# Optimization experiments

Measured on AMD Instinct MI355X. Metric: run time of the kernel, lower is better.

## Reference

```python
import jax, jax.numpy as jnp
import numpy as np

N = 100_000      # nodes
E = 1_600_000    # edges (avg degree 16)
D = 64           # input_dim == hidden_dim
C = 10           # output classes
G = 512          # graphs in batch
L = 5            # num_layers (L-1 = 4 GINConv layers)
BN_EPS = 1e-5


def setup_inputs() -> dict:
    key = jax.random.key(0)
    ks = jax.random.split(key, 16)
    x = jax.random.normal(ks[0], (N, D), dtype=jnp.float32)
    edge_index = jax.random.randint(ks[1], (2, E), 0, N, dtype=jnp.int32)
    batch = jnp.sort(jax.random.randint(ks[2], (N,), 0, G, dtype=jnp.int32))
    s = 1.0 / np.sqrt(D)
    Lc = L - 1
    return {
        "x": x,
        "edge_index": edge_index,
        "batch": batch,
        "eps": jnp.zeros((Lc,), jnp.float32),                                   # GINConv eps (train_eps, init 0)
        "W1": jax.random.uniform(ks[3], (Lc, D, D), jnp.float32, -s, s),        # MLP linear 1
        "b1": jax.random.uniform(ks[4], (Lc, D), jnp.float32, -s, s),
        "g1": jnp.ones((Lc, D), jnp.float32),                                   # MLP BatchNorm
        "be1": jnp.zeros((Lc, D), jnp.float32),
        "W2": jax.random.uniform(ks[5], (Lc, D, D), jnp.float32, -s, s),        # MLP linear 2
        "b2": jax.random.uniform(ks[6], (Lc, D), jnp.float32, -s, s),
        "gout": jnp.ones((Lc, D), jnp.float32),                                 # outer BatchNorm
        "beout": jnp.zeros((Lc, D), jnp.float32),
        "Wp": jax.random.uniform(ks[7], (L, D, C), jnp.float32, -s, s),         # prediction linears
        "bp": jax.random.uniform(ks[8], (L, C), jnp.float32, -s, s),
    }


def _batchnorm(h, gamma, beta):
    # training-mode BN over node dim, biased variance (torch semantics)
    m = jnp.mean(h, axis=0)
    v = jnp.mean(jnp.square(h - m), axis=0)
    return gamma * (h - m) * jax.lax.rsqrt(v + BN_EPS) + beta


def reference(x, edge_index, batch, eps, W1, b1, g1, be1, W2, b2, gout, beout, Wp, bp):
    src, dst = edge_index[0], edge_index[1]
    hidden_rep = [x]
    h = x
    for l in range(L - 1):
        # GINConv: (1 + eps) * x + scatter-add of neighbor features
        agg = jax.ops.segment_sum(h[src], dst, num_segments=N)
        z = (1.0 + eps[l]) * h + agg
        # 2-layer MLP with internal BN+ReLU
        z = z @ W1[l] + b1[l]
        z = jax.nn.relu(_batchnorm(z, g1[l], be1[l]))
        z = z @ W2[l] + b2[l]
        # outer BN + ReLU
        h = jax.nn.relu(_batchnorm(z, gout[l], beout[l]))
        hidden_rep.append(h)
    # jumping-knowledge readout: per-layer global_add_pool + linear (dropout off / eval)
    score = jnp.zeros((G, C), jnp.float32)
    for l, hl in enumerate(hidden_rep):
        pooled = jax.ops.segment_sum(hl, batch, num_segments=G)
        score = score + pooled @ Wp[l] + bp[l]
    return score
```

## Files before the change

### kernel.cpp

```cpp
#include <hip/hip_runtime.h>

#define NN 100000
#define EE 1600000
#define DD 64
#define CC 10
#define GG 512
#define LL 5
#define NPAD 100352
#define N64 (NN * DD)
#define NB 392
#define PCH 4096
#define BCAP 6144
#define SC 8

typedef short bf16x8 __attribute__((ext_vector_type(8)));
typedef float f32x4  __attribute__((ext_vector_type(4)));
union U16 { uint4 u; bf16x8 h; };

__device__ __forceinline__ float bits2f(unsigned int b) { return __uint_as_float(b); }
__device__ __forceinline__ float bf2f(unsigned short s) { return __uint_as_float((unsigned int)s << 16); }
__device__ __forceinline__ unsigned short f2bf_rne(float v) {
    unsigned int b = __float_as_uint(v);
    return (unsigned short)((b + 0x7fffu + ((b >> 16) & 1u)) >> 16);
}
__device__ __forceinline__ void unpack8(uint4 u, float* f) {
    f[0] = bits2f(u.x << 16); f[1] = bits2f(u.x & 0xffff0000u);
    f[2] = bits2f(u.y << 16); f[3] = bits2f(u.y & 0xffff0000u);
    f[4] = bits2f(u.z << 16); f[5] = bits2f(u.z & 0xffff0000u);
    f[6] = bits2f(u.w << 16); f[7] = bits2f(u.w & 0xffff0000u);
}
__device__ __forceinline__ uint4 pack8(const float* f) {
    uint4 u;
    u.x = (unsigned int)f2bf_rne(f[0]) | ((unsigned int)f2bf_rne(f[1]) << 16);
    u.y = (unsigned int)f2bf_rne(f[2]) | ((unsigned int)f2bf_rne(f[3]) << 16);
    u.z = (unsigned int)f2bf_rne(f[4]) | ((unsigned int)f2bf_rne(f[5]) << 16);
    u.w = (unsigned int)f2bf_rne(f[6]) | ((unsigned int)f2bf_rne(f[7]) << 16);
    return u;
}

__global__ __launch_bounds__(256) void prep_x_pool_k(
    const float* __restrict__ x, const int* __restrict__ batch,
    unsigned short* __restrict__ hb, float* __restrict__ pooled)
{
    int t = threadIdx.x;
    int f = t & 63;
    int q = t >> 6;
    int n0 = blockIdx.x * 64 + q * 16;
    int nmax = NN - n0; if (nmax > 16) nmax = 16;
    float acc = 0.f;
    int curg = -1;
    #pragma unroll 4
    for (int i = 0; i < nmax; ++i) {
        int n = n0 + i;
        int g = batch[n];
        if (g != curg) {
            if (curg >= 0) atomicAdd(&pooled[(size_t)curg * DD + f], acc);
            acc = 0.f; curg = g;
        }
        float v = x[(size_t)n * DD + f];
        hb[(size_t)n * DD + f] = f2bf_rne(v);
        acc += v;
    }
    if (curg >= 0) atomicAdd(&pooled[(size_t)curg * DD + f], acc);
}

__global__ __launch_bounds__(256) void prep_w_k(const float* __restrict__ W1,
                                                const float* __restrict__ W2,
                                                unsigned short* __restrict__ wt) {
    int mat = blockIdx.x;
    const float* src = (mat < 4) ? (W1 + (size_t)mat * 4096)
                                 : (W2 + (size_t)(mat - 4) * 4096);
    for (int idx = threadIdx.x; idx < 4096; idx += 256) {
        int c = idx >> 6, k = idx & 63;
        wt[(size_t)mat * 4096 + c * 64 + k] = f2bf_rne(src[k * 64 + c]);
    }
}

__global__ __launch_bounds__(256) void bhist_k(const int* __restrict__ ei,
                                               int* __restrict__ bh) {
    __shared__ int cnt[NB];
    for (int i = threadIdx.x; i < NB; i += 256) cnt[i] = 0;
    __syncthreads();
    int stride = gridDim.x * 256;
    for (int e = blockIdx.x * 256 + threadIdx.x; e < EE; e += stride)
        atomicAdd(&cnt[ei[EE + e] >> 8], 1);
    __syncthreads();
    for (int i = threadIdx.x; i < NB; i += 256)
        if (cnt[i]) atomicAdd(&bh[i], cnt[i]);
}

__global__ __launch_bounds__(512) void bscan_k(const int* __restrict__ bh,
                                               int* __restrict__ bo,
                                               int* __restrict__ bcur) {
    __shared__ int s[512];
    int t = threadIdx.x;
    int v = (t < NB) ? bh[t] : 0;
    s[t] = v;
    __syncthreads();
    for (int d = 1; d < 512; d <<= 1) {
        int a = (t >= d) ? s[t - d] : 0;
        __syncthreads();
        s[t] += a;
        __syncthreads();
    }
    int excl = s[t] - v;
    if (t < NB) { bo[t] = excl; bcur[t] = excl; }
    if (t == NB - 1) bo[NB] = excl + v;
}

__global__ __launch_bounds__(256) void partition_k(const int* __restrict__ ei,
                                                   int* __restrict__ bcur,
                                                   uint2* __restrict__ stage) {
    __shared__ int hist[NB];
    __shared__ int base[NB];
    __shared__ int gbase[NB];
    __shared__ int cnt2[NB];
    __shared__ int scanbuf[512];
    __shared__ uint2 pairs[PCH];
    int t = threadIdx.x;
    int e0 = blockIdx.x * PCH;
    int nE = EE - e0; if (nE > PCH) nE = PCH;

    for (int i = t; i < NB; i += 256) { hist[i] = 0; cnt2[i] = 0; }
    __syncthreads();

    int mys[16], myd[16];
    #pragma unroll
    for (int i = 0; i < 16; ++i) {
        int idx = i * 256 + t;
        if (idx < nE) {
            mys[i] = ei[e0 + idx];
            myd[i] = ei[EE + e0 + idx];
            atomicAdd(&hist[myd[i] >> 8], 1);
        } else myd[i] = -1;
    }
    __syncthreads();

    scanbuf[t]       = (t < NB) ? hist[t] : 0;
    scanbuf[t + 256] = (t + 256 < NB) ? hist[t + 256] : 0;
    __syncthreads();
    for (int d = 1; d < 512; d <<= 1) {
        int a0 = (t >= d) ? scanbuf[t - d] : 0;
        int a1 = ((t + 256) >= d) ? scanbuf[t + 256 - d] : 0;
        __syncthreads();
        scanbuf[t] += a0;
        scanbuf[t + 256] += a1;
        __syncthreads();
    }
    if (t < NB)       base[t]       = scanbuf[t] - hist[t];
    if (t + 256 < NB) base[t + 256] = scanbuf[t + 256] - hist[t + 256];
    __syncthreads();

    #pragma unroll
    for (int i = 0; i < 16; ++i) {
        if (myd[i] >= 0) {
            int b = myd[i] >> 8;
            int p = base[b] + atomicAdd(&cnt2[b], 1);
            pairs[p] = make_uint2((unsigned)mys[i], (unsigned)myd[i]);
        }
    }
    __syncthreads();
    for (int i = t; i < NB; i += 256)
        if (hist[i]) gbase[i] = atomicAdd(&bcur[i], hist[i]);
    __syncthreads();
    for (int p = t; p < nE; p += 256) {
        uint2 pr = pairs[p];
        int b = (int)(pr.y >> 8);
        stage[gbase[b] + (p - base[b])] = pr;
    }
}

__global__ __launch_bounds__(256) void bucket_csr_k(const uint2* __restrict__ stage,
                                                    const int* __restrict__ bo,
                                                    int* __restrict__ adj,
                                                    int* __restrict__ offs) {
    __shared__ int deg[256];
    __shared__ int sb[256];
    __shared__ int nb_[256];
    __shared__ int c2[256];
    __shared__ int loc[BCAP];
    int b = blockIdx.x;
    int s0 = bo[b], s1 = bo[b + 1];
    int cnt = s1 - s0;
    int t = threadIdx.x;

    deg[t] = 0;
    __syncthreads();
    for (int i = t; i < cnt; i += 256) atomicAdd(&deg[stage[s0 + i].y & 255], 1);
    __syncthreads();
    sb[t] = deg[t];
    __syncthreads();
    for (int d = 1; d < 256; d <<= 1) {
        int a = (t >= d) ? sb[t - d] : 0;
        __syncthreads();
        sb[t] += a;
        __syncthreads();
    }
    int nbase = sb[t] - deg[t];
    nb_[t] = nbase;
    c2[t] = 0;
    offs[b * 256 + t] = s0 + nbase;
    __syncthreads();

    if (cnt <= BCAP) {
        for (int i = t; i < cnt; i += 256) {
            uint2 pr = stage[s0 + i];
            int ln = pr.y & 255;
            int p = nb_[ln] + atomicAdd(&c2[ln], 1);
            loc[p] = (int)pr.x;
        }
        __syncthreads();
        for (int i = t; i < cnt; i += 256) adj[s0 + i] = loc[i];
    } else {
        for (int i = t; i < cnt; i += 256) {
            uint2 pr = stage[s0 + i];
            int ln = pr.y & 255;
            int p = nb_[ln] + atomicAdd(&c2[ln], 1);
            adj[s0 + p] = (int)pr.x;
        }
    }
}

__global__ __launch_bounds__(256) void layer1_k(
    const unsigned short* __restrict__ hb, const int* __restrict__ adj,
    const int* __restrict__ offs, const float* __restrict__ epsArr, int l,
    const unsigned short* __restrict__ wtm, const float* __restrict__ bias,
    unsigned short* __restrict__ z1, float* __restrict__ stats1,
    float* __restrict__ stats2z)
{
    __shared__ unsigned short aLDS[64 * 64];
    const int t = threadIdx.x;
    const int lane = t & 63;
    const int w = t >> 6;
    const int n15 = lane & 15;
    const int quad = lane >> 4;

    if (blockIdx.x < SC && t < 128) stats2z[blockIdx.x * 128 + t] = 0.f;

    const float epsv = 1.0f + epsArr[l];
    const int c8 = lane & 7;
    #pragma unroll
    for (int it = 0; it < 2; ++it) {
        int lr = w * 16 + it * 8 + (lane >> 3);
        int n = blockIdx.x * 64 + lr;
        float acc[8] = {0.f,0.f,0.f,0.f,0.f,0.f,0.f,0.f};
        if (n < NN) {
            float tmp[8];
            uint4 a = *(const uint4*)(hb + (size_t)n * DD + c8 * 8);
            unpack8(a, acc);
            #pragma unroll
            for (int j2 = 0; j2 < 8; ++j2) acc[j2] *= epsv;
            int j = offs[n], end = offs[n + 1];
            for (; j + 3 < end; j += 4) {
                int s0 = adj[j], s1 = adj[j + 1], s2 = adj[j + 2], s3 = adj[j + 3];
                uint4 v0 = *(const uint4*)(hb + (size_t)s0 * DD + c8 * 8);
                uint4 v1 = *(const uint4*)(hb + (size_t)s1 * DD + c8 * 8);
                uint4 v2 = *(const uint4*)(hb + (size_t)s2 * DD + c8 * 8);
                uint4 v3 = *(const uint4*)(hb + (size_t)s3 * DD + c8 * 8);
                unpack8(v0, tmp);
                #pragma unroll
                for (int k2 = 0; k2 < 8; ++k2) acc[k2] += tmp[k2];
                unpack8(v1, tmp);
                #pragma unroll
                for (int k2 = 0; k2 < 8; ++k2) acc[k2] += tmp[k2];
                unpack8(v2, tmp);
                #pragma unroll
                for (int k2 = 0; k2 < 8; ++k2) acc[k2] += tmp[k2];
                unpack8(v3, tmp);
                #pragma unroll
                for (int k2 = 0; k2 < 8; ++k2) acc[k2] += tmp[k2];
            }
            for (; j < end; ++j) {
                uint4 v0 = *(const uint4*)(hb + (size_t)adj[j] * DD + c8 * 8);
                unpack8(v0, tmp);
                #pragma unroll
                for (int k2 = 0; k2 < 8; ++k2) acc[k2] += tmp[k2];
            }
        }
        int pu = c8 ^ (lr & 7);
        *(uint4*)(aLDS + lr * 64 + pu * 8) = pack8(acc);
    }

    U16 afr[2];
    int lr2 = w * 16 + n15;
    #pragma unroll
    for (int ks = 0; ks < 2; ++ks) {
        int pu = (ks * 4 + quad) ^ (lr2 & 7);
        afr[ks].u = *(const uint4*)(aLDS + lr2 * 64 + pu * 8);
    }
    U16 bfr[4][2];
    #pragma unroll
    for (int ct = 0; ct < 4; ++ct)
        #pragma unroll
        for (int ks = 0; ks < 2; ++ks)
            bfr[ct][ks].u = *(const uint4*)(wtm + (size_t)(ct * 16 + n15) * 64 + ks * 32 + quad * 8);

    const int rowg0 = blockIdx.x * 64 + w * 16;
    const int copy = blockIdx.x & (SC - 1);
    #pragma unroll
    for (int ct = 0; ct < 4; ++ct) {
        f32x4 acc = {0.f, 0.f, 0.f, 0.f};
        acc = __builtin_amdgcn_mfma_f32_16x16x32_bf16(afr[0].h, bfr[ct][0].h, acc, 0, 0, 0);
        acc = __builtin_amdgcn_mfma_f32_16x16x32_bf16(afr[1].h, bfr[ct][1].h, acc, 0, 0, 0);
        int col = ct * 16 + n15;
        float bcol = bias[col];
        float s = 0.f, ss = 0.f;
        #pragma unroll
        for (int r = 0; r < 4; ++r) {
            int rg = rowg0 + quad * 4 + r;
            float v = acc[r] + bcol;
            if (rg < NN) {
                z1[(size_t)rg * DD + col] = f2bf_rne(v);
                s += v;
                ss = fmaf(v, v, ss);
            }
        }
        s  += __shfl_xor(s, 16, 64);  s  += __shfl_xor(s, 32, 64);
        ss += __shfl_xor(ss, 16, 64); ss += __shfl_xor(ss, 32, 64);
        if (lane < 16) {
            atomicAdd(&stats1[copy * 128 + ct * 16 + lane], s);
            atomicAdd(&stats1[copy * 128 + 64 + ct * 16 + lane], ss);
        }
    }
}

__global__ __launch_bounds__(256) void layer2_k(
    const unsigned short* __restrict__ z1, const float* __restrict__ stats1,
    const float* __restrict__ gamma, const float* __restrict__ beta, int off,
    const unsigned short* __restrict__ wtm, const float* __restrict__ bias,
    unsigned short* __restrict__ z2, float* __restrict__ stats2)
{
    __shared__ float ssS[128];
    const int t = threadIdx.x;
    if (t < 64) {
        float S = 0.f, SS = 0.f;
        #pragma unroll
        for (int c = 0; c < SC; ++c) { S += stats1[c * 128 + t]; SS += stats1[c * 128 + 64 + t]; }
        float inv_n = 1.0f / (float)NN;
        float mean = S * inv_n;
        float var  = SS * inv_n - mean * mean;
        float sc = gamma[off + t] * rsqrtf(var + 1e-5f);
        ssS[t] = sc;
        ssS[64 + t] = beta[off + t] - sc * mean;
    }
    __syncthreads();

    const int lane = t & 63;
    const int w = t >> 6;
    const int n15 = lane & 15;
    const int quad = lane >> 4;
    const int rowg0 = blockIdx.x * 64 + w * 16;

    U16 bfr[4][2];
    #pragma unroll
    for (int ct = 0; ct < 4; ++ct)
        #pragma unroll
        for (int ks = 0; ks < 2; ++ks)
            bfr[ct][ks].u = *(const uint4*)(wtm + (size_t)(ct * 16 + n15) * 64 + ks * 32 + quad * 8);

    U16 afr[2];
    int arow = rowg0 + n15;
    int arowc = (arow < NN) ? arow : (NN - 1);
    #pragma unroll
    for (int ks = 0; ks < 2; ++ks) {
        uint4 raw = *(const uint4*)(z1 + (size_t)arowc * DD + ks * 32 + quad * 8);
        float f[8];
        unpack8(raw, f);
        int k0 = ks * 32 + quad * 8;
        #pragma unroll
        for (int j = 0; j < 8; ++j)
            f[j] = fmaxf(fmaf(ssS[k0 + j], f[j], ssS[64 + k0 + j]), 0.f);
        afr[ks].u = pack8(f);
    }

    const int copy = blockIdx.x & (SC - 1);
    #pragma unroll
    for (int ct = 0; ct < 4; ++ct) {
        f32x4 acc = {0.f, 0.f, 0.f, 0.f};
        acc = __builtin_amdgcn_mfma_f32_16x16x32_bf16(afr[0].h, bfr[ct][0].h, acc, 0, 0, 0);
        acc = __builtin_amdgcn_mfma_f32_16x16x32_bf16(afr[1].h, bfr[ct][1].h, acc, 0, 0, 0);
        int col = ct * 16 + n15;
        float bcol = bias[col];
        float s = 0.f, ss = 0.f;
        #pragma unroll
        for (int r = 0; r < 4; ++r) {
            int rg = rowg0 + quad * 4 + r;
            float v = acc[r] + bcol;
            if (rg < NN) {
                z2[(size_t)rg * DD + col] = f2bf_rne(v);
                s += v;
                ss = fmaf(v, v, ss);
            }
        }
        s  += __shfl_xor(s, 16, 64);  s  += __shfl_xor(s, 32, 64);
        ss += __shfl_xor(ss, 16, 64); ss += __shfl_xor(ss, 32, 64);
        if (lane < 16) {
            atomicAdd(&stats2[copy * 128 + ct * 16 + lane], s);
            atomicAdd(&stats2[copy * 128 + 64 + ct * 16 + lane], ss);
        }
    }
}

__global__ __launch_bounds__(256) void layer3_k(
    const unsigned short* __restrict__ z2, const float* __restrict__ stats2,
    const float* __restrict__ gamma, const float* __restrict__ beta, int off,
    const int* __restrict__ batch, unsigned short* __restrict__ hout,
    float* __restrict__ pooled, float* __restrict__ stats1z)
{
    __shared__ float ssS[128];
    int t = threadIdx.x;
    if (blockIdx.x < SC && t < 128) stats1z[blockIdx.x * 128 + t] = 0.f;
    if (t < 64) {
        float S = 0.f, SS = 0.f;
        #pragma unroll
        for (int c = 0; c < SC; ++c) { S += stats2[c * 128 + t]; SS += stats2[c * 128 + 64 + t]; }
        float inv_n = 1.0f / (float)NN;
        float mean = S * inv_n;
        float var  = SS * inv_n - mean * mean;
        float sc = gamma[off + t] * rsqrtf(var + 1e-5f);
        ssS[t] = sc;
        ssS[64 + t] = beta[off + t] - sc * mean;
    }
    __syncthreads();

    int f = t & 63;
    int q = t >> 6;
    int n0 = blockIdx.x * 64 + q * 16;
    int nmax = NN - n0; if (nmax > 16) nmax = 16;
    float sc = ssS[f], sh = ssS[64 + f];
    float acc = 0.f;
    int curg = -1;
    #pragma unroll 4
    for (int i = 0; i < nmax; ++i) {
        int n = n0 + i;
        int g = batch[n];
        if (g != curg) {
            if (curg >= 0) atomicAdd(&pooled[(size_t)curg * DD + f], acc);
            acc = 0.f; curg = g;
        }
        float v = bf2f(z2[(size_t)n * DD + f]);
        v = fmaxf(fmaf(sc, v, sh), 0.f);
        hout[(size_t)n * DD + f] = f2bf_rne(v);
        acc += v;
    }
    if (curg >= 0) atomicAdd(&pooled[(size_t)curg * DD + f], acc);
}

__global__ void readout_k(const float* __restrict__ pooled,
                          const float* __restrict__ Wp, const float* __restrict__ bp,
                          float* __restrict__ out)
{
    int gc = blockIdx.x * blockDim.x + threadIdx.x;
    if (gc >= GG * CC) return;
    int g = gc / CC, c = gc - g * CC;
    float acc = 0.f;
    for (int l = 0; l < LL; ++l) {
        acc += bp[l * CC + c];
        const float* p  = pooled + ((size_t)l * GG + g) * DD;
        const float* wv = Wp + (size_t)l * DD * CC + c;
        #pragma unroll 8
        for (int f = 0; f < DD; ++f) acc = fmaf(p[f], wv[f * CC], acc);
    }
    out[gc] = acc;
}

extern "C" void kernel_launch(void* const* d_in, const int* in_sizes, int n_in,
                              void* d_out, int out_size, void* d_ws, size_t ws_size,
                              hipStream_t stream) {
    const float* x     = (const float*)d_in[0];
    const int*   ei    = (const int*)d_in[1];
    const int*   batch = (const int*)d_in[2];
    const float* eps   = (const float*)d_in[3];
    const float* W1    = (const float*)d_in[4];
    const float* b1    = (const float*)d_in[5];
    const float* g1    = (const float*)d_in[6];
    const float* be1   = (const float*)d_in[7];
    const float* W2    = (const float*)d_in[8];
    const float* b2    = (const float*)d_in[9];
    const float* gout  = (const float*)d_in[10];
    const float* beout = (const float*)d_in[11];
    const float* Wp    = (const float*)d_in[12];
    const float* bp    = (const float*)d_in[13];
    float* out = (float*)d_out;

    uint2* stage = (uint2*)d_ws;
    int* adj   = (int*)(stage + EE);
    int* offs  = adj + EE;
    int* bh    = offs + NPAD + 256;
    int* bo    = bh + 400;
    int* bcur  = bo + 400;
    float* pooled = (float*)(bcur + 400);
    float* stats1 = pooled + (size_t)LL * GG * DD;
    float* stats2 = stats1 + SC * 128;
    unsigned short* hb  = (unsigned short*)(stats2 + SC * 128);
    unsigned short* z1b = hb + N64;
    unsigned short* z2b = z1b + N64;
    unsigned short* wt  = z2b + N64;

    hipMemsetAsync(pooled, 0, ((size_t)LL * GG * DD + 2 * SC * 128) * sizeof(float), stream);
    prep_x_pool_k<<<(NN + 63) / 64, 256, 0, stream>>>(x, batch, hb, pooled);
    prep_w_k<<<8, 256, 0, stream>>>(W1, W2, wt);

    hipMemsetAsync(bh, 0, NB * sizeof(int), stream);
    bhist_k<<<512, 256, 0, stream>>>(ei, bh);
    bscan_k<<<1, 512, 0, stream>>>(bh, bo, bcur);
    partition_k<<<(EE + PCH - 1) / PCH, 256, 0, stream>>>(ei, bcur, stage);
    bucket_csr_k<<<NB, 256, 0, stream>>>(stage, bo, adj, offs);

    const int gemm_grid = (NN + 63) / 64;
    const int node_grid = (NN + 63) / 64;
    for (int l = 0; l < LL - 1; ++l) {
        layer1_k<<<gemm_grid, 256, 0, stream>>>(
            hb, adj, offs, eps, l, wt + (size_t)l * 4096, b1 + l * DD, z1b, stats1, stats2);
        layer2_k<<<gemm_grid, 256, 0, stream>>>(
            z1b, stats1, g1, be1, l * DD, wt + (size_t)(4 + l) * 4096, b2 + l * DD, z2b, stats2);
        layer3_k<<<node_grid, 256, 0, stream>>>(
            z2b, stats2, gout, beout, l * DD, batch, hb,
            pooled + (size_t)(l + 1) * GG * DD, stats1);
    }
    readout_k<<<(GG * CC + 255) / 256, 256, 0, stream>>>(pooled, Wp, bp, out);
}
```

Before: 653.7 us.

## Pack partition staging into 32-bit words and gather rows one node per wave

The edge staging buffer is shrunk from 8-byte (src,dst) pairs to one 32-bit word holding the 17-bit source and the 8-bit local destination. The bucket is recovered by binary search over the prefix scan, which halves global and shared traffic in partitioning and CSR build. The layer1 aggregation is restructured so a whole wave handles one node: each lane gathers one bf16 feature, and neighbour indices are loaded 16 at a time and broadcast with readlane. This trades wide 16-byte vector loads for 2-byte scalar loads per lane and serialises nodes within a wave, which may raise the number of memory instructions.

```diff
diff --git a/kernel.cpp b/kernel.cpp
--- a/kernel.cpp
+++ b/kernel.cpp
@@ -110,13 +110,13 @@
 
 __global__ __launch_bounds__(256) void partition_k(const int* __restrict__ ei,
                                                    int* __restrict__ bcur,
-                                                   uint2* __restrict__ stage) {
+                                                   unsigned int* __restrict__ stage) {
     __shared__ int hist[NB];
     __shared__ int base[NB];
     __shared__ int gbase[NB];
     __shared__ int cnt2[NB];
     __shared__ int scanbuf[512];
-    __shared__ uint2 pairs[PCH];
+    __shared__ unsigned int pairs[PCH];
     int t = threadIdx.x;
     int e0 = blockIdx.x * PCH;
     int nE = EE - e0; if (nE > PCH) nE = PCH;
@@ -156,7 +156,7 @@
         if (myd[i] >= 0) {
             int b = myd[i] >> 8;
             int p = base[b] + atomicAdd(&cnt2[b], 1);
-            pairs[p] = make_uint2((unsigned)mys[i], (unsigned)myd[i]);
+            pairs[p] = (unsigned)mys[i] | ((unsigned)(myd[i] & 255) << 17);
         }
     }
     __syncthreads();
@@ -164,13 +164,19 @@
         if (hist[i]) gbase[i] = atomicAdd(&bcur[i], hist[i]);
     __syncthreads();
     for (int p = t; p < nE; p += 256) {
-        uint2 pr = pairs[p];
-        int b = (int)(pr.y >> 8);
+        unsigned int pr = pairs[p];
+        int b = -1;
+        int lo = 0, hi = NB - 1;
+        while (lo < hi) {
+            int mid = (lo + hi) >> 1;
+            if (p < scanbuf[mid]) hi = mid; else lo = mid + 1;
+        }
+        b = lo;
         stage[gbase[b] + (p - base[b])] = pr;
     }
 }
 
-__global__ __launch_bounds__(256) void bucket_csr_k(const uint2* __restrict__ stage,
+__global__ __launch_bounds__(256) void bucket_csr_k(const unsigned int* __restrict__ stage,
                                                     const int* __restrict__ bo,
                                                     int* __restrict__ adj,
                                                     int* __restrict__ offs) {
@@ -186,7 +192,7 @@
 
     deg[t] = 0;
     __syncthreads();
-    for (int i = t; i < cnt; i += 256) atomicAdd(&deg[stage[s0 + i].y & 255], 1);
+    for (int i = t; i < cnt; i += 256) atomicAdd(&deg[(stage[s0 + i] >> 17) & 255], 1);
     __syncthreads();
     sb[t] = deg[t];
     __syncthreads();
@@ -204,19 +210,19 @@
 
     if (cnt <= BCAP) {
         for (int i = t; i < cnt; i += 256) {
-            uint2 pr = stage[s0 + i];
-            int ln = pr.y & 255;
+            unsigned int pr = stage[s0 + i];
+            int ln = (pr >> 17) & 255;
             int p = nb_[ln] + atomicAdd(&c2[ln], 1);
-            loc[p] = (int)pr.x;
+            loc[p] = (int)(pr & 0x1FFFF);
         }
         __syncthreads();
         for (int i = t; i < cnt; i += 256) adj[s0 + i] = loc[i];
     } else {
         for (int i = t; i < cnt; i += 256) {
-            uint2 pr = stage[s0 + i];
-            int ln = pr.y & 255;
+            unsigned int pr = stage[s0 + i];
+            int ln = (pr >> 17) & 255;
             int p = nb_[ln] + atomicAdd(&c2[ln], 1);
-            adj[s0 + p] = (int)pr.x;
+            adj[s0 + p] = (int)(pr & 0x1FFFF);
         }
     }
 }
@@ -238,47 +244,31 @@
     if (blockIdx.x < SC && t < 128) stats2z[blockIdx.x * 128 + t] = 0.f;
 
     const float epsv = 1.0f + epsArr[l];
-    const int c8 = lane & 7;
-    #pragma unroll
-    for (int it = 0; it < 2; ++it) {
-        int lr = w * 16 + it * 8 + (lane >> 3);
+
+    for (int i = 0; i < 16; ++i) {
+        int lr = w * 16 + i;
         int n = blockIdx.x * 64 + lr;
-        float acc[8] = {0.f,0.f,0.f,0.f,0.f,0.f,0.f,0.f};
+        float acc = 0.f;
         if (n < NN) {
-            float tmp[8];
-            uint4 a = *(const uint4*)(hb + (size_t)n * DD + c8 * 8);
-            unpack8(a, acc);
-            #pragma unroll
-            for (int j2 = 0; j2 < 8; ++j2) acc[j2] *= epsv;
-            int j = offs[n], end = offs[n + 1];
-            for (; j + 3 < end; j += 4) {
-                int s0 = adj[j], s1 = adj[j + 1], s2 = adj[j + 2], s3 = adj[j + 3];
-                uint4 v0 = *(const uint4*)(hb + (size_t)s0 * DD + c8 * 8);
-                uint4 v1 = *(const uint4*)(hb + (size_t)s1 * DD + c8 * 8);
-                uint4 v2 = *(const uint4*)(hb + (size_t)s2 * DD + c8 * 8);
-                uint4 v3 = *(const uint4*)(hb + (size_t)s3 * DD + c8 * 8);
-                unpack8(v0, tmp);
+            acc = epsv * bf2f(hb[(size_t)n * DD + lane]);
+            int j = __builtin_amdgcn_readfirstlane(offs[n]);
+            int end = __builtin_amdgcn_readfirstlane(offs[n + 1]);
+            while (j < end) {
+                int cnt = end - j; if (cnt > 16) cnt = 16;
+                int idx = j + n15; if (idx >= end) idx = end - 1;
+                int myadj = adj[idx];
                 #pragma unroll
-                for (int k2 = 0; k2 < 8; ++k2) acc[k2] += tmp[k2];
-                unpack8(v1, tmp);
-                #pragma unroll
-                for (int k2 = 0; k2 < 8; ++k2) acc[k2] += tmp[k2];
-                unpack8(v2, tmp);
-                #pragma unroll
-                for (int k2 = 0; k2 < 8; ++k2) acc[k2] += tmp[k2];
-                unpack8(v3, tmp);
-                #pragma unroll
-                for (int k2 = 0; k2 < 8; ++k2) acc[k2] += tmp[k2];
+                for (int k = 0; k < 16; ++k) {
+                    if (k < cnt) {
+                        int s = __builtin_amdgcn_readlane(myadj, k);
+                        acc += bf2f(hb[(size_t)s * DD + lane]);
+                    }
+                }
+                j += cnt;
             }
-            for (; j < end; ++j) {
-                uint4 v0 = *(const uint4*)(hb + (size_t)adj[j] * DD + c8 * 8);
-                unpack8(v0, tmp);
-                #pragma unroll
-                for (int k2 = 0; k2 < 8; ++k2) acc[k2] += tmp[k2];
-            }
-        }
-        int pu = c8 ^ (lr & 7);
-        *(uint4*)(aLDS + lr * 64 + pu * 8) = pack8(acc);
+        }
+        int u = (lane >> 3) ^ (lr & 7);
+        aLDS[lr * 64 + u * 8 + (lane & 7)] = f2bf_rne(acc);
     }
 
     U16 afr[2];
@@ -483,7 +473,7 @@
     const float* bp    = (const float*)d_in[13];
     float* out = (float*)d_out;
 
-    uint2* stage = (uint2*)d_ws;
+    unsigned int* stage = (unsigned int*)d_ws;
     int* adj   = (int*)(stage + EE);
     int* offs  = adj + EE;
     int* bh    = offs + NPAD + 256;
```

After: 889.9 us. +36.1%, slower.
